# Optimization experiments

Hardware: AMD Instinct MI355X
Metric: run time of the kernel (lower is better)

## Reference

```python
import jax, jax.numpy as jnp
import numpy as np

N_ATOMS = 100000
N_BONDS = 200000
N_MOLS = 4000
ATOMS_PER_MOL = 25
MAX_NB = 6
ATOM_FDIM = 133
BOND_FDIM = 14
HIDDEN = 300
DEPTH = 3


def setup_inputs() -> dict:
    key = jax.random.key(0)
    ks = jax.random.split(key, 8)
    f_atoms = jax.random.normal(ks[0], (N_ATOMS, ATOM_FDIM), dtype=jnp.float32)
    f_bonds = jax.random.normal(ks[1], (N_BONDS, BOND_FDIM), dtype=jnp.float32)
    # incoming-bond lists per atom (irregular gather targets)
    a2b = jax.random.randint(ks[2], (N_ATOMS, MAX_NB), 0, N_BONDS, dtype=jnp.int32)
    # source atom of each directed bond
    b2a = jax.random.randint(ks[3], (N_BONDS,), 0, N_ATOMS, dtype=jnp.int32)
    # reverse bond: directed bonds come in pairs (2i, 2i+1)
    b2revb = (jnp.arange(N_BONDS, dtype=jnp.int32) ^ 1)
    # contiguous [start, size] per molecule
    starts = jnp.arange(N_MOLS, dtype=jnp.int32) * ATOMS_PER_MOL
    sizes = jnp.full((N_MOLS,), ATOMS_PER_MOL, dtype=jnp.int32)
    a_scope = jnp.stack([starts, sizes], axis=1)
    W_i = jax.random.normal(ks[4], (HIDDEN, ATOM_FDIM + BOND_FDIM), dtype=jnp.float32) * 0.05
    W_h = jax.random.normal(ks[5], (HIDDEN, HIDDEN), dtype=jnp.float32) * 0.05
    W_o = jax.random.normal(ks[6], (HIDDEN, ATOM_FDIM + HIDDEN), dtype=jnp.float32) * 0.05
    b_o = jax.random.normal(ks[7], (HIDDEN,), dtype=jnp.float32) * 0.05
    return {"f_atoms": f_atoms, "f_bonds": f_bonds, "a2b": a2b, "b2a": b2a,
            "b2revb": b2revb, "a_scope": a_scope, "W_i": W_i, "W_h": W_h,
            "W_o": W_o, "b_o": b_o}


def reference(f_atoms, f_bonds, a2b, b2a, b2revb, a_scope, W_i, W_h, W_o, b_o):
    # initial directed-bond messages: [f_atoms[src], f_bonds] -> Linear -> ReLU
    input_feats = jnp.concatenate([f_atoms[b2a], f_bonds], axis=1)  # (E, 147)
    message = jax.nn.relu(input_feats @ W_i.T)  # (E, H)
    for _ in range(DEPTH - 1):
        nei_a_message = message[a2b].sum(axis=1)          # (V, H) gather+sum
        nei_message = nei_a_message[b2a] - message[b2revb]  # (E, H)
        message = jax.nn.relu(nei_message @ W_h.T)
    a_message = message[a2b].sum(axis=1)  # (V, H)
    atom_hiddens = jax.nn.relu(jnp.concatenate([f_atoms, a_message], axis=1) @ W_o.T + b_o)
    # vectorized scope mean-pool (scopes are contiguous ranges)
    starts = a_scope[:, 0]
    sizes = a_scope[:, 1]
    seg_ids = jnp.searchsorted(starts, jnp.arange(atom_hiddens.shape[0]), side='right') - 1
    sums = jax.ops.segment_sum(atom_hiddens, seg_ids, num_segments=N_MOLS)
    denom = jnp.maximum(sizes, 1).astype(atom_hiddens.dtype)[:, None]
    mol_vecs = jnp.where((sizes > 0)[:, None], sums / denom, 0.0)
    return mol_vecs
```

## Files before the change

kernel.cpp:

```cpp
#include <hip/hip_runtime.h>
#include <hip/hip_bf16.h>
#include <stdint.h>

#define N_ATOMS   100000
#define N_BONDS   200000
#define N_MOLS    4000
#define MAX_NB    6
#define ATOM_FDIM 133
#define BOND_FDIM 14
#define HIDDEN    300
#define NPAD      320
#define KPAD_I    160
#define KPAD_H    320
#define KPAD_O    448

typedef __attribute__((ext_vector_type(8))) short          bf16x8;
typedef __attribute__((ext_vector_type(8))) unsigned short u16x8;
typedef __attribute__((ext_vector_type(4))) float          f32x4;

__device__ __forceinline__ float bf2f(unsigned short u) {
  union { unsigned int i; float f; } v; v.i = ((unsigned int)u) << 16; return v.f;
}
__device__ __forceinline__ unsigned short f2bf(float f) {
  union { float f; unsigned int i; } v; v.f = f;
  unsigned int u = v.i;
  return (unsigned short)((u + 0x7fffu + ((u >> 16) & 1u)) >> 16);
}

__global__ void convw_kernel(const float* __restrict__ w, unsigned short* __restrict__ o,
                             int N, int K, int KP) {
  int total = NPAD * KP;
  for (int idx = blockIdx.x * 256 + threadIdx.x; idx < total; idx += gridDim.x * 256) {
    int n = idx / KP, k = idx - n * KP;
    float v = (n < N && k < K) ? w[n * K + k] : 0.f;
    o[idx] = f2bf(v);
  }
}

__global__ void agg_kernel(const unsigned short* __restrict__ msg,
                           const int* __restrict__ a2b,
                           unsigned short* __restrict__ nei) {
  int idx = blockIdx.x * 256 + threadIdx.x;
  const int total = N_ATOMS * (NPAD / 8);
  if (idx >= total) return;
  int a  = idx / (NPAD / 8);
  int kc = (idx - a * (NPAD / 8)) * 8;
  float s[8];
#pragma unroll
  for (int e = 0; e < 8; e++) s[e] = 0.f;
#pragma unroll
  for (int j = 0; j < MAX_NB; j++) {
    int b = a2b[a * MAX_NB + j];
    u16x8 v = *(const u16x8*)&msg[(size_t)b * NPAD + kc];
#pragma unroll
    for (int e = 0; e < 8; e++) s[e] += bf2f(v[e]);
  }
  u16x8 o;
#pragma unroll
  for (int e = 0; e < 8; e++) o[e] = f2bf(s[e]);
  *(u16x8*)&nei[(size_t)a * NPAD + kc] = o;
}

template<int SRC>
__device__ __forceinline__ u16x8 stage_load(
    int ks, int q, int row, int gatherRow, int revRow,
    const float* __restrict__ f_atoms, const float* __restrict__ f_bonds,
    const unsigned short* __restrict__ nei, const unsigned short* msgin) {
  const int kc = ks * 32 + q * 8;
  u16x8 r;
  if (SRC == 1) {
    u16x8 n8 = *(const u16x8*)&nei[(size_t)gatherRow * NPAD + kc];
    u16x8 m8 = *(const u16x8*)&msgin[(size_t)revRow * NPAD + kc];
#pragma unroll
    for (int j = 0; j < 8; j++) r[j] = f2bf(bf2f(n8[j]) - bf2f(m8[j]));
  } else if (SRC == 0) {
#pragma unroll
    for (int j = 0; j < 8; j++) {
      int k = kc + j; float v = 0.f;
      if (k < ATOM_FDIM)                  v = f_atoms[(size_t)gatherRow * ATOM_FDIM + k];
      else if (k < ATOM_FDIM + BOND_FDIM) v = f_bonds[(size_t)row * BOND_FDIM + (k - ATOM_FDIM)];
      r[j] = f2bf(v);
    }
  } else {
#pragma unroll
    for (int j = 0; j < 8; j++) {
      int k = kc + j; float v = 0.f;
      if (k < ATOM_FDIM)               v = f_atoms[(size_t)row * ATOM_FDIM + k];
      else if (k < ATOM_FDIM + HIDDEN) v = bf2f(nei[(size_t)row * NPAD + (k - ATOM_FDIM)]);
      r[j] = f2bf(v);
    }
  }
  return r;
}

template<int SRC>
__global__ __launch_bounds__(256, 2) void gemm64_kernel(
    const float* __restrict__ f_atoms, const float* __restrict__ f_bonds,
    const int* __restrict__ b2a, const int* __restrict__ b2revb,
    const unsigned short* __restrict__ nei,
    const unsigned short* msgin,
    const unsigned short* __restrict__ W,
    const float* __restrict__ bias,
    unsigned short* out, int M) {
  constexpr int KP  = (SRC == 0) ? KPAD_I : (SRC == 1) ? KPAD_H : KPAD_O;
  constexpr int NST = KP / 32;
  __shared__ __align__(16) unsigned short As[NST * 2048];

  const int b0   = blockIdx.x * 64;
  const int tid  = threadIdx.x;
  const int lane = tid & 63;
  const int wave = tid >> 6;
  const int sr   = tid >> 2;
  const int q    = tid & 3;

  int row = b0 + sr;
  if (row >= M) row = M - 1;
  int gatherRow = 0, revRow = 0;
  if (SRC == 0 || SRC == 1) gatherRow = b2a[row];
  if (SRC == 1) revRow = b2revb[row];

  const int dbase = (sr >> 4) * 512 + (q * 16 + (sr & 15)) * 8;

  constexpr int G = 5;
#pragma unroll
  for (int ks0 = 0; ks0 < NST; ks0 += G) {
    u16x8 vals[G];
#pragma unroll
    for (int j = 0; j < G; j++) {
      const int ks = ks0 + j;
      if (ks < NST)
        vals[j] = stage_load<SRC>(ks, q, row, gatherRow, revRow, f_atoms, f_bonds, nei, msgin);
    }
#pragma unroll
    for (int j = 0; j < G; j++) {
      const int ks = ks0 + j;
      if (ks < NST) *(u16x8*)&As[ks * 2048 + dbase] = vals[j];
    }
  }
  __syncthreads();

  f32x4 acc[4][5];
#pragma unroll
  for (int m = 0; m < 4; m++)
#pragma unroll
    for (int n = 0; n < 5; n++) acc[m][n] = (f32x4){0.f, 0.f, 0.f, 0.f};

  const int nbase = wave * 80;
  const unsigned short* Wl = W + (size_t)(nbase + (lane & 15)) * KP + ((lane >> 4) * 8);

#pragma unroll
  for (int ks = 0; ks < NST; ks++) {
    bf16x8 afrag[4];
#pragma unroll
    for (int m = 0; m < 4; m++)
      afrag[m] = *(const bf16x8*)&As[ks * 2048 + m * 512 + lane * 8];
#pragma unroll
    for (int nf = 0; nf < 5; nf++) {
      bf16x8 bfrag = *(const bf16x8*)(Wl + (size_t)nf * 16 * KP + ks * 32);
#pragma unroll
      for (int m = 0; m < 4; m++)
        acc[m][nf] = __builtin_amdgcn_mfma_f32_16x16x32_bf16(afrag[m], bfrag, acc[m][nf], 0, 0, 0);
    }
  }

#pragma unroll
  for (int m = 0; m < 4; m++) {
#pragma unroll
    for (int r = 0; r < 4; r++) {
      int orow = b0 + m * 16 + (lane >> 4) * 4 + r;
      if (orow >= M) continue;
#pragma unroll
      for (int nf = 0; nf < 5; nf++) {
        int ocol = nbase + nf * 16 + (lane & 15);
        float v = acc[m][nf][r];
        if (SRC == 2) v += (ocol < HIDDEN) ? bias[ocol] : 0.f;
        v = v > 0.f ? v : 0.f;
        out[(size_t)orow * NPAD + ocol] = f2bf(v);
      }
    }
  }
}

__global__ void readout_kernel(const unsigned short* __restrict__ hidden,
                               const int* __restrict__ a_scope,
                               float* __restrict__ out) {
  int idx = blockIdx.x * 256 + threadIdx.x;
  const int total = N_MOLS * HIDDEN;
  if (idx >= total) return;
  int m = idx / HIDDEN, c = idx - m * HIDDEN;
  int start = a_scope[m * 2], size = a_scope[m * 2 + 1];
  float s = 0.f;
  for (int i = 0; i < size; i++) s += bf2f(hidden[(size_t)(start + i) * NPAD + c]);
  out[idx] = (size > 0) ? s / (float)size : 0.f;
}

extern "C" void kernel_launch(void* const* d_in, const int* in_sizes, int n_in,
                              void* d_out, int out_size, void* d_ws, size_t ws_size,
                              hipStream_t stream) {
  const float* f_atoms = (const float*)d_in[0];
  const float* f_bonds = (const float*)d_in[1];
  const int*   a2b     = (const int*)d_in[2];
  const int*   b2a     = (const int*)d_in[3];
  const int*   b2revb  = (const int*)d_in[4];
  const int*   a_scope = (const int*)d_in[5];
  const float* W_i     = (const float*)d_in[6];
  const float* W_h     = (const float*)d_in[7];
  const float* W_o     = (const float*)d_in[8];
  const float* b_o     = (const float*)d_in[9];
  float* out = (float*)d_out;

  char* ws = (char*)d_ws;
  size_t off = 0;
  auto alloc = [&](size_t bytes) { size_t o = off; off += (bytes + 255) & ~(size_t)255; return o; };
  unsigned short* msg    = (unsigned short*)(ws + alloc((size_t)N_BONDS * NPAD * 2));
  unsigned short* nei    = (unsigned short*)(ws + alloc((size_t)N_ATOMS * NPAD * 2));
  unsigned short* hidden = (unsigned short*)(ws + alloc((size_t)N_ATOMS * NPAD * 2));
  unsigned short* Wi_bf  = (unsigned short*)(ws + alloc((size_t)NPAD * KPAD_I * 2));
  unsigned short* Wh_bf  = (unsigned short*)(ws + alloc((size_t)NPAD * KPAD_H * 2));
  unsigned short* Wo_bf  = (unsigned short*)(ws + alloc((size_t)NPAD * KPAD_O * 2));

  convw_kernel<<<(NPAD * KPAD_I + 255) / 256, 256, 0, stream>>>(W_i, Wi_bf, HIDDEN, ATOM_FDIM + BOND_FDIM, KPAD_I);
  convw_kernel<<<(NPAD * KPAD_H + 255) / 256, 256, 0, stream>>>(W_h, Wh_bf, HIDDEN, HIDDEN, KPAD_H);
  convw_kernel<<<(NPAD * KPAD_O + 255) / 256, 256, 0, stream>>>(W_o, Wo_bf, HIDDEN, ATOM_FDIM + HIDDEN, KPAD_O);

  const int gb = N_BONDS / 64;
  const int ga = (N_ATOMS + 63) / 64;

  gemm64_kernel<0><<<gb, 256, 0, stream>>>(f_atoms, f_bonds, b2a, b2revb, nullptr, nullptr,
                                           Wi_bf, nullptr, msg, N_BONDS);
  for (int d = 0; d < 2; d++) {
    agg_kernel<<<(N_ATOMS * (NPAD / 8)) / 256, 256, 0, stream>>>(msg, a2b, nei);
    gemm64_kernel<1><<<gb, 256, 0, stream>>>(f_atoms, f_bonds, b2a, b2revb, nei, msg,
                                             Wh_bf, nullptr, msg, N_BONDS);
  }
  agg_kernel<<<(N_ATOMS * (NPAD / 8)) / 256, 256, 0, stream>>>(msg, a2b, nei);
  gemm64_kernel<2><<<ga, 256, 0, stream>>>(f_atoms, f_bonds, b2a, b2revb, nei, nullptr,
                                           Wo_bf, b_o, hidden, N_ATOMS);
  readout_kernel<<<(N_MOLS * HIDDEN + 255) / 256, 256, 0, stream>>>(hidden, a_scope, out);
}
```

Before: 730.4 us.

## Load GEMM A-fragments directly from global memory, dropping LDS staging

```diff
diff --git a/kernel.cpp b/kernel.cpp
--- a/kernel.cpp
+++ b/kernel.cpp
@@ -10,91 +10,79 @@
 #define BOND_FDIM 14
 #define HIDDEN    300
 #define NPAD      320
-#define KPAD_I    160
+#define KPAD_I    192
 #define KPAD_H    320
-#define KPAD_O    448
+#define KPAD_O    480
+#define SEG2_OFF  160
 
 typedef __attribute__((ext_vector_type(8))) short          bf16x8;
-typedef __attribute__((ext_vector_type(8))) unsigned short u16x8;
 typedef __attribute__((ext_vector_type(4))) float          f32x4;
-
-__device__ __forceinline__ float bf2f(unsigned short u) {
-  union { unsigned int i; float f; } v; v.i = ((unsigned int)u) << 16; return v.f;
-}
-__device__ __forceinline__ unsigned short f2bf(float f) {
-  union { float f; unsigned int i; } v; v.f = f;
-  unsigned int u = v.i;
+typedef __attribute__((ext_vector_type(4))) unsigned int   u32x4;
+typedef __attribute__((ext_vector_type(4), aligned(4))) float f32x4u;
+
+static __device__ __forceinline__ float u2f(unsigned int u) {
+  union { unsigned int u; float f; } v; v.u = u; return v.f;
+}
+static __device__ __forceinline__ unsigned int f2u(float f) {
+  union { float f; unsigned int u; } v; v.f = f; return v.u;
+}
+static __device__ __forceinline__ unsigned int pack_bf(float lo, float hi) {
+  return __builtin_amdgcn_perm(f2u(hi), f2u(lo), 0x07060302u);
+}
+static __device__ __forceinline__ float bf2f(unsigned short u) {
+  return u2f(((unsigned int)u) << 16);
+}
+static __device__ __forceinline__ unsigned short f2bf_rn(float f) {
+  unsigned int u = f2u(f);
   return (unsigned short)((u + 0x7fffu + ((u >> 16) & 1u)) >> 16);
 }
 
 __global__ void convw_kernel(const float* __restrict__ w, unsigned short* __restrict__ o,
-                             int N, int K, int KP) {
+                             int K, int seg1, int seg2len, int KP) {
   int total = NPAD * KP;
   for (int idx = blockIdx.x * 256 + threadIdx.x; idx < total; idx += gridDim.x * 256) {
     int n = idx / KP, k = idx - n * KP;
-    float v = (n < N && k < K) ? w[n * K + k] : 0.f;
-    o[idx] = f2bf(v);
+    int src = -1;
+    if (k < seg1) src = k;
+    else if (k >= SEG2_OFF && k < SEG2_OFF + seg2len) src = k - (SEG2_OFF - seg1);
+    float v = (n < HIDDEN && src >= 0) ? w[n * K + src] : 0.f;
+    o[idx] = f2bf_rn(v);
   }
 }
 
 __global__ void agg_kernel(const unsigned short* __restrict__ msg,
                            const int* __restrict__ a2b,
                            unsigned short* __restrict__ nei) {
+  const int TPA = NPAD / 16;
   int idx = blockIdx.x * 256 + threadIdx.x;
-  const int total = N_ATOMS * (NPAD / 8);
-  if (idx >= total) return;
-  int a  = idx / (NPAD / 8);
-  int kc = (idx - a * (NPAD / 8)) * 8;
-  float s[8];
-#pragma unroll
-  for (int e = 0; e < 8; e++) s[e] = 0.f;
+  if (idx >= N_ATOMS * TPA) return;
+  int a  = idx / TPA;
+  int kc = (idx - a * TPA) * 16;
+  int bidx[MAX_NB];
+#pragma unroll
+  for (int j = 0; j < MAX_NB; j++) bidx[j] = a2b[a * MAX_NB + j];
+  float slo[8], shi[8];
+#pragma unroll
+  for (int t = 0; t < 8; t++) { slo[t] = 0.f; shi[t] = 0.f; }
 #pragma unroll
   for (int j = 0; j < MAX_NB; j++) {
-    int b = a2b[a * MAX_NB + j];
-    u16x8 v = *(const u16x8*)&msg[(size_t)b * NPAD + kc];
-#pragma unroll
-    for (int e = 0; e < 8; e++) s[e] += bf2f(v[e]);
-  }
-  u16x8 o;
-#pragma unroll
-  for (int e = 0; e < 8; e++) o[e] = f2bf(s[e]);
-  *(u16x8*)&nei[(size_t)a * NPAD + kc] = o;
+    const u32x4* p = (const u32x4*)(msg + (size_t)bidx[j] * NPAD + kc);
+    u32x4 v0 = p[0], v1 = p[1];
+#pragma unroll
+    for (int t = 0; t < 4; t++) {
+      slo[t]     += u2f(v0[t] << 16); shi[t]     += u2f(v0[t] & 0xffff0000u);
+      slo[4 + t] += u2f(v1[t] << 16); shi[4 + t] += u2f(v1[t] & 0xffff0000u);
+    }
+  }
+  u32x4 o0, o1;
+#pragma unroll
+  for (int t = 0; t < 4; t++) { o0[t] = pack_bf(slo[t], shi[t]); o1[t] = pack_bf(slo[4 + t], shi[4 + t]); }
+  u32x4* q = (u32x4*)(nei + (size_t)a * NPAD + kc);
+  q[0] = o0; q[1] = o1;
 }
 
 template<int SRC>
-__device__ __forceinline__ u16x8 stage_load(
-    int ks, int q, int row, int gatherRow, int revRow,
-    const float* __restrict__ f_atoms, const float* __restrict__ f_bonds,
-    const unsigned short* __restrict__ nei, const unsigned short* msgin) {
-  const int kc = ks * 32 + q * 8;
-  u16x8 r;
-  if (SRC == 1) {
-    u16x8 n8 = *(const u16x8*)&nei[(size_t)gatherRow * NPAD + kc];
-    u16x8 m8 = *(const u16x8*)&msgin[(size_t)revRow * NPAD + kc];
-#pragma unroll
-    for (int j = 0; j < 8; j++) r[j] = f2bf(bf2f(n8[j]) - bf2f(m8[j]));
-  } else if (SRC == 0) {
-#pragma unroll
-    for (int j = 0; j < 8; j++) {
-      int k = kc + j; float v = 0.f;
-      if (k < ATOM_FDIM)                  v = f_atoms[(size_t)gatherRow * ATOM_FDIM + k];
-      else if (k < ATOM_FDIM + BOND_FDIM) v = f_bonds[(size_t)row * BOND_FDIM + (k - ATOM_FDIM)];
-      r[j] = f2bf(v);
-    }
-  } else {
-#pragma unroll
-    for (int j = 0; j < 8; j++) {
-      int k = kc + j; float v = 0.f;
-      if (k < ATOM_FDIM)               v = f_atoms[(size_t)row * ATOM_FDIM + k];
-      else if (k < ATOM_FDIM + HIDDEN) v = bf2f(nei[(size_t)row * NPAD + (k - ATOM_FDIM)]);
-      r[j] = f2bf(v);
-    }
-  }
-  return r;
-}
-
-template<int SRC>
-__global__ __launch_bounds__(256, 2) void gemm64_kernel(
+__global__ __launch_bounds__(256) void gemm64_kernel(
     const float* __restrict__ f_atoms, const float* __restrict__ f_bonds,
     const int* __restrict__ b2a, const int* __restrict__ b2revb,
     const unsigned short* __restrict__ nei,
@@ -104,40 +92,23 @@
     unsigned short* out, int M) {
   constexpr int KP  = (SRC == 0) ? KPAD_I : (SRC == 1) ? KPAD_H : KPAD_O;
   constexpr int NST = KP / 32;
-  __shared__ __align__(16) unsigned short As[NST * 2048];
 
   const int b0   = blockIdx.x * 64;
   const int tid  = threadIdx.x;
   const int lane = tid & 63;
   const int wave = tid >> 6;
-  const int sr   = tid >> 2;
-  const int q    = tid & 3;
-
-  int row = b0 + sr;
-  if (row >= M) row = M - 1;
-  int gatherRow = 0, revRow = 0;
-  if (SRC == 0 || SRC == 1) gatherRow = b2a[row];
-  if (SRC == 1) revRow = b2revb[row];
-
-  const int dbase = (sr >> 4) * 512 + (q * 16 + (sr & 15)) * 8;
-
-  constexpr int G = 5;
-#pragma unroll
-  for (int ks0 = 0; ks0 < NST; ks0 += G) {
-    u16x8 vals[G];
-#pragma unroll
-    for (int j = 0; j < G; j++) {
-      const int ks = ks0 + j;
-      if (ks < NST)
-        vals[j] = stage_load<SRC>(ks, q, row, gatherRow, revRow, f_atoms, f_bonds, nei, msgin);
-    }
-#pragma unroll
-    for (int j = 0; j < G; j++) {
-      const int ks = ks0 + j;
-      if (ks < NST) *(u16x8*)&As[ks * 2048 + dbase] = vals[j];
-    }
-  }
-  __syncthreads();
+  const int kq   = lane >> 4;
+  const int ar   = lane & 15;
+
+  int rowm[4], g[4], r[4];
+#pragma unroll
+  for (int m = 0; m < 4; m++) {
+    int row = b0 + m * 16 + ar;
+    if (row >= M) row = M - 1;
+    rowm[m] = row;
+    if (SRC == 0) g[m] = b2a[row];
+    if (SRC == 1) { g[m] = b2a[row]; r[m] = b2revb[row]; }
+  }
 
   f32x4 acc[4][5];
 #pragma unroll
@@ -146,36 +117,83 @@
     for (int n = 0; n < 5; n++) acc[m][n] = (f32x4){0.f, 0.f, 0.f, 0.f};
 
   const int nbase = wave * 80;
-  const unsigned short* Wl = W + (size_t)(nbase + (lane & 15)) * KP + ((lane >> 4) * 8);
+  const unsigned short* Wl = W + (size_t)(nbase + ar) * KP + kq * 8;
+
+  auto load_frag = [&](int m, int ks) -> bf16x8 {
+    union { u32x4 u; bf16x8 h; } cv;
+    if (SRC == 1) {
+      const int off = ks * 32 + kq * 8;
+      u32x4 n8 = *(const u32x4*)(nei   + (size_t)g[m] * NPAD + off);
+      u32x4 m8 = *(const u32x4*)(msgin + (size_t)r[m] * NPAD + off);
+#pragma unroll
+      for (int t = 0; t < 4; t++) {
+        float d0 = u2f(n8[t] << 16)        - u2f(m8[t] << 16);
+        float d1 = u2f(n8[t] & 0xffff0000u) - u2f(m8[t] & 0xffff0000u);
+        cv.u[t] = pack_bf(d0, d1);
+      }
+      return cv.h;
+    }
+    if (SRC == 2 && ks >= 5) {
+      cv.u = *(const u32x4*)(nei + (size_t)rowm[m] * NPAD + (ks - 5) * 32 + kq * 8);
+      return cv.h;
+    }
+    const int arow = (SRC == 0) ? g[m] : rowm[m];
+    if (ks <= 3) {
+      const float* pa = f_atoms + (size_t)arow * ATOM_FDIM + ks * 32 + kq * 8;
+      f32x4u v0 = *(const f32x4u*)pa;
+      f32x4u v1 = *(const f32x4u*)(pa + 4);
+      cv.u[0] = pack_bf(v0[0], v0[1]); cv.u[1] = pack_bf(v0[2], v0[3]);
+      cv.u[2] = pack_bf(v1[0], v1[1]); cv.u[3] = pack_bf(v1[2], v1[3]);
+      return cv.h;
+    }
+    float v[8];
+    if (ks == 4) {
+#pragma unroll
+      for (int j = 0; j < 8; j++) {
+        int k = 128 + kq * 8 + j;
+        v[j] = (k < ATOM_FDIM) ? f_atoms[(size_t)arow * ATOM_FDIM + k] : 0.f;
+      }
+    } else {
+#pragma unroll
+      for (int j = 0; j < 8; j++) {
+        int k2 = kq * 8 + j;
+        v[j] = (k2 < BOND_FDIM) ? f_bonds[(size_t)rowm[m] * BOND_FDIM + k2] : 0.f;
+      }
+    }
+    cv.u[0] = pack_bf(v[0], v[1]); cv.u[1] = pack_bf(v[2], v[3]);
+    cv.u[2] = pack_bf(v[4], v[5]); cv.u[3] = pack_bf(v[6], v[7]);
+    return cv.h;
+  };
 
 #pragma unroll
   for (int ks = 0; ks < NST; ks++) {
-    bf16x8 afrag[4];
-#pragma unroll
-    for (int m = 0; m < 4; m++)
-      afrag[m] = *(const bf16x8*)&As[ks * 2048 + m * 512 + lane * 8];
+    bf16x8 af[4];
+#pragma unroll
+    for (int m = 0; m < 4; m++) af[m] = load_frag(m, ks);
 #pragma unroll
     for (int nf = 0; nf < 5; nf++) {
-      bf16x8 bfrag = *(const bf16x8*)(Wl + (size_t)nf * 16 * KP + ks * 32);
+      bf16x8 bfr = *(const bf16x8*)(Wl + (size_t)nf * 16 * KP + ks * 32);
 #pragma unroll
       for (int m = 0; m < 4; m++)
-        acc[m][nf] = __builtin_amdgcn_mfma_f32_16x16x32_bf16(afrag[m], bfrag, acc[m][nf], 0, 0, 0);
-    }
-  }
+        acc[m][nf] = __builtin_amdgcn_mfma_f32_16x16x32_bf16(af[m], bfr, acc[m][nf], 0, 0, 0);
+    }
+  }
+
+  if (SRC == 1) __syncthreads();
 
 #pragma unroll
   for (int m = 0; m < 4; m++) {
 #pragma unroll
-    for (int r = 0; r < 4; r++) {
-      int orow = b0 + m * 16 + (lane >> 4) * 4 + r;
+    for (int rr = 0; rr < 4; rr++) {
+      int orow = b0 + m * 16 + (lane >> 4) * 4 + rr;
       if (orow >= M) continue;
 #pragma unroll
       for (int nf = 0; nf < 5; nf++) {
-        int ocol = nbase + nf * 16 + (lane & 15);
-        float v = acc[m][nf][r];
-        if (SRC == 2) v += (ocol < HIDDEN) ? bias[ocol] : 0.f;
-        v = v > 0.f ? v : 0.f;
-        out[(size_t)orow * NPAD + ocol] = f2bf(v);
+        int ocol = nbase + nf * 16 + ar;
+        float vv = acc[m][nf][rr];
+        if (SRC == 2) vv += (ocol < HIDDEN) ? bias[ocol] : 0.f;
+        vv = vv > 0.f ? vv : 0.f;
+        out[(size_t)orow * NPAD + ocol] = f2bf_rn(vv);
       }
     }
   }
@@ -219,21 +237,22 @@
   unsigned short* Wh_bf  = (unsigned short*)(ws + alloc((size_t)NPAD * KPAD_H * 2));
   unsigned short* Wo_bf  = (unsigned short*)(ws + alloc((size_t)NPAD * KPAD_O * 2));
 
-  convw_kernel<<<(NPAD * KPAD_I + 255) / 256, 256, 0, stream>>>(W_i, Wi_bf, HIDDEN, ATOM_FDIM + BOND_FDIM, KPAD_I);
-  convw_kernel<<<(NPAD * KPAD_H + 255) / 256, 256, 0, stream>>>(W_h, Wh_bf, HIDDEN, HIDDEN, KPAD_H);
-  convw_kernel<<<(NPAD * KPAD_O + 255) / 256, 256, 0, stream>>>(W_o, Wo_bf, HIDDEN, ATOM_FDIM + HIDDEN, KPAD_O);
+  convw_kernel<<<(NPAD * KPAD_I + 255) / 256, 256, 0, stream>>>(W_i, Wi_bf, ATOM_FDIM + BOND_FDIM, ATOM_FDIM, BOND_FDIM, KPAD_I);
+  convw_kernel<<<(NPAD * KPAD_H + 255) / 256, 256, 0, stream>>>(W_h, Wh_bf, HIDDEN, HIDDEN, 0, KPAD_H);
+  convw_kernel<<<(NPAD * KPAD_O + 255) / 256, 256, 0, stream>>>(W_o, Wo_bf, ATOM_FDIM + HIDDEN, ATOM_FDIM, HIDDEN, KPAD_O);
 
   const int gb = N_BONDS / 64;
   const int ga = (N_ATOMS + 63) / 64;
+  const int gagg = (N_ATOMS * (NPAD / 16) + 255) / 256;
 
   gemm64_kernel<0><<<gb, 256, 0, stream>>>(f_atoms, f_bonds, b2a, b2revb, nullptr, nullptr,
                                            Wi_bf, nullptr, msg, N_BONDS);
   for (int d = 0; d < 2; d++) {
-    agg_kernel<<<(N_ATOMS * (NPAD / 8)) / 256, 256, 0, stream>>>(msg, a2b, nei);
+    agg_kernel<<<gagg, 256, 0, stream>>>(msg, a2b, nei);
     gemm64_kernel<1><<<gb, 256, 0, stream>>>(f_atoms, f_bonds, b2a, b2revb, nei, msg,
                                              Wh_bf, nullptr, msg, N_BONDS);
   }
-  agg_kernel<<<(N_ATOMS * (NPAD / 8)) / 256, 256, 0, stream>>>(msg, a2b, nei);
+  agg_kernel<<<gagg, 256, 0, stream>>>(msg, a2b, nei);
   gemm64_kernel<2><<<ga, 256, 0, stream>>>(f_atoms, f_bonds, b2a, b2revb, nei, nullptr,
                                            Wo_bf, b_o, hidden, N_ATOMS);
   readout_kernel<<<(N_MOLS * HIDDEN + 255) / 256, 256, 0, stream>>>(hidden, a_scope, out);
```

New measurement: 930.7 us. +27.4%, slower.
